# Performance work log

Hardware: AMD Instinct MI355X
Metric: run time of the kernel (lower is better)

Reference implementation:

```python
import jax, jax.numpy as jnp
import numpy as np

BN_EPS = 1e-5


def sparsemax(z):
    # z: [B, D]; sparse projection onto the simplex along last axis.
    D = z.shape[-1]
    z_sorted = jnp.flip(jnp.sort(z, axis=-1), axis=-1)          # descending
    cs = jnp.cumsum(z_sorted, axis=-1)                           # cumulative sums
    k = jnp.arange(1, D + 1, dtype=z.dtype)                      # 1..D
    support = (1.0 + k * z_sorted) > cs                          # support condition
    k_star = jnp.sum(support, axis=-1, keepdims=True)            # support size, int
    cs_k = jnp.take_along_axis(cs, k_star - 1, axis=-1)
    tau = (cs_k - 1.0) / k_star.astype(z.dtype)                  # threshold
    return jnp.maximum(z - tau, 0.0)


def setup_inputs() -> dict:
    key = jax.random.key(0)
    k1, k2, k3 = jax.random.split(key, 3)
    B, D = 32768, 1024
    a = jax.random.normal(k1, (B, D), dtype=jnp.float32)
    p = jax.random.uniform(k2, (B, D), dtype=jnp.float32)        # prior scales in (0,1)
    W = jax.random.normal(k3, (D, D), dtype=jnp.float32) * (1.0 / np.sqrt(D))
    b = jnp.zeros((D,), dtype=jnp.float32)
    gamma = jnp.ones((D,), dtype=jnp.float32)
    beta = jnp.zeros((D,), dtype=jnp.float32)
    return {"a": a, "p": p, "W": W, "b": b, "gamma": gamma, "beta": beta}


def reference(a, p, W, b, gamma, beta):
    # Linear: a @ W^T + b  (torch nn.Linear convention)
    h = jnp.einsum("bd,ed->be", a, W) + b
    # BatchNorm1d (training mode: batch stats, biased variance)
    mean = jnp.mean(h, axis=0)
    var = jnp.mean(jnp.square(h - mean), axis=0)
    h = (h - mean) * jax.lax.rsqrt(var + BN_EPS) * gamma + beta
    # Prior scaling, then sparsemax -> attention mask
    mask = sparsemax(p * h)
    return mask
```

## Files before the change

kernel.cpp:

```cpp
#include <hip/hip_runtime.h>
#include <hip/hip_fp16.h>
#include <stdint.h>

typedef _Float16 f16x8 __attribute__((ext_vector_type(8)));
typedef _Float16 f16x2 __attribute__((ext_vector_type(2)));
typedef float f32x4 __attribute__((ext_vector_type(4)));

#define BM 128
#define BN 128
#define BK 64

__device__ __forceinline__ void async_copy16(const void* g, void* l) {
  __builtin_amdgcn_global_load_lds(
      (__attribute__((address_space(1))) void*)(g),
      (__attribute__((address_space(3))) void*)(l),
      16, 0, 0);
}

__global__ __launch_bounds__(256) void cvt_f32_f16(const float* __restrict__ in,
                                                   _Float16* __restrict__ out,
                                                   size_t n) {
  size_t i = ((size_t)blockIdx.x * 256 + threadIdx.x) * 8;
  if (i + 8 > n) return;
  float4 u = *(const float4*)(in + i);
  float4 v = *(const float4*)(in + i + 4);
  f16x8 h;
  h[0] = (_Float16)u.x; h[1] = (_Float16)u.y; h[2] = (_Float16)u.z; h[3] = (_Float16)u.w;
  h[4] = (_Float16)v.x; h[5] = (_Float16)v.y; h[6] = (_Float16)v.z; h[7] = (_Float16)v.w;
  *(f16x8*)(out + i) = h;
}

template <bool H16>
__global__ __launch_bounds__(256) void gemm_direct(const _Float16* __restrict__ Ah,
                                                   const _Float16* __restrict__ Wh,
                                                   const float* __restrict__ bias,
                                                   void* __restrict__ Hout,
                                                   float* __restrict__ psum,
                                                   float* __restrict__ psumsq,
                                                   int M, int N, int K) {
  __shared__ __attribute__((aligned(16))) _Float16 lsA[BM * BK];
  __shared__ __attribute__((aligned(16))) _Float16 lsB[BN * BK];

  const int tid  = threadIdx.x;
  const int wave = tid >> 6;
  const int lane = tid & 63;
  const int wrow = (wave >> 1) * 64;
  const int wcol = (wave & 1) * 64;
  const int l16  = lane & 15;
  const int quad = lane >> 4;

  const int nx = gridDim.x;
  const int li = blockIdx.y * nx + blockIdx.x;
  const int xcd = li & 7;
  const int jj  = li >> 3;
  const int bnT = jj % nx;
  const int bmT = xcd + (jj / nx) * 8;
  const int bm = bmT * BM;
  const int bn = bnT * BN;

  f32x4 acc[4][4];
#pragma unroll
  for (int i = 0; i < 4; ++i)
#pragma unroll
    for (int j = 0; j < 4; ++j) acc[i][j] = (f32x4){0.f, 0.f, 0.f, 0.f};

  for (int k0 = 0; k0 < K; k0 += BK) {
#pragma unroll
    for (int i = 0; i < 4; ++i) {
      const int basechunk = i * 256 + wave * 64;
      const int g   = basechunk + lane;
      const int row = g >> 3;
      const int kc  = ((g & 7) ^ (row & 7)) << 3;
      async_copy16(Ah + (size_t)(bm + row) * K + k0 + kc, &lsA[basechunk * 8]);
      async_copy16(Wh + (size_t)(bn + row) * K + k0 + kc, &lsB[basechunk * 8]);
    }
    __syncthreads();

#pragma unroll
    for (int kk = 0; kk < BK; kk += 32) {
      f16x8 af[4], bf[4];
#pragma unroll
      for (int i = 0; i < 4; ++i) {
        const int r = wrow + i * 16 + l16;
        const int col = ((kk >> 3) + quad) ^ (l16 & 7);
        af[i] = *(const f16x8*)&lsA[r * 64 + col * 8];
      }
#pragma unroll
      for (int j = 0; j < 4; ++j) {
        const int r = wcol + j * 16 + l16;
        const int col = ((kk >> 3) + quad) ^ (l16 & 7);
        bf[j] = *(const f16x8*)&lsB[r * 64 + col * 8];
      }
#pragma unroll
      for (int i = 0; i < 4; ++i)
#pragma unroll
        for (int j = 0; j < 4; ++j)
          acc[i][j] = __builtin_amdgcn_mfma_f32_16x16x32_f16(af[i], bf[j], acc[i][j], 0, 0, 0);
    }
    __syncthreads();
  }

#pragma unroll
  for (int j = 0; j < 4; ++j) {
    const int c = bn + wcol + j * 16 + l16;
    const float bv = bias[c];
    float s = 0.f, s2 = 0.f;
#pragma unroll
    for (int i = 0; i < 4; ++i) {
      const int r = bm + wrow + i * 16 + quad * 4;
      f32x4 v = acc[i][j];
      const float v0 = v[0] + bv, v1 = v[1] + bv, v2 = v[2] + bv, v3 = v[3] + bv;
      s += v0 + v1 + v2 + v3;
      s2 += v0 * v0 + v1 * v1 + v2 * v2 + v3 * v3;
      if constexpr (H16) {
        f16x2* H2 = (f16x2*)Hout;
        const size_t d0 = (size_t)(r >> 1) * N + c;
        H2[d0]     = (f16x2){(_Float16)v0, (_Float16)v1};
        H2[d0 + N] = (f16x2){(_Float16)v2, (_Float16)v3};
      } else {
        float* Cp = (float*)Hout + (size_t)r * N + c;
        Cp[0] = v0; Cp[(size_t)N] = v1; Cp[2 * (size_t)N] = v2; Cp[3 * (size_t)N] = v3;
      }
    }
    s  += __shfl_xor(s, 16, 64);  s  += __shfl_xor(s, 32, 64);
    s2 += __shfl_xor(s2, 16, 64); s2 += __shfl_xor(s2, 32, 64);
    if (quad == 0) {
      const size_t slot = (size_t)(bmT * 2 + (wave >> 1)) * N + c;
      psum[slot] = s;
      psumsq[slot] = s2;
    }
  }
}

__global__ __launch_bounds__(256) void gemm_fallback(const float* __restrict__ Af,
                                                     const float* __restrict__ Wf,
                                                     const float* __restrict__ bias,
                                                     float* __restrict__ C,
                                                     float* __restrict__ sum,
                                                     float* __restrict__ sumsq,
                                                     int M, int N, int K) {
  __shared__ __attribute__((aligned(16))) _Float16 lsA[BM * BK];
  __shared__ __attribute__((aligned(16))) _Float16 lsB[BN * BK];
  const int tid  = threadIdx.x;
  const int wave = tid >> 6;
  const int lane = tid & 63;
  const int wrow = (wave >> 1) * 64;
  const int wcol = (wave & 1) * 64;
  const int l16  = lane & 15;
  const int quad = lane >> 4;
  const int bm = blockIdx.y * BM;
  const int bn = blockIdx.x * BN;

  f32x4 acc[4][4];
#pragma unroll
  for (int i = 0; i < 4; ++i)
#pragma unroll
    for (int j = 0; j < 4; ++j) acc[i][j] = (f32x4){0.f, 0.f, 0.f, 0.f};

  for (int k0 = 0; k0 < K; k0 += BK) {
#pragma unroll
    for (int i = 0; i < 4; ++i) {
      const int g   = i * 256 + tid;
      const int row = g >> 3;
      const int kc  = ((g & 7) ^ (row & 7)) << 3;
      {
        const float* src = Af + (size_t)(bm + row) * K + k0 + kc;
        float4 u = *(const float4*)src;
        float4 v = *(const float4*)(src + 4);
        f16x8 h;
        h[0] = (_Float16)u.x; h[1] = (_Float16)u.y; h[2] = (_Float16)u.z; h[3] = (_Float16)u.w;
        h[4] = (_Float16)v.x; h[5] = (_Float16)v.y; h[6] = (_Float16)v.z; h[7] = (_Float16)v.w;
        *(f16x8*)&lsA[g * 8] = h;
      }
      {
        const float* src = Wf + (size_t)(bn + row) * K + k0 + kc;
        float4 u = *(const float4*)src;
        float4 v = *(const float4*)(src + 4);
        f16x8 h;
        h[0] = (_Float16)u.x; h[1] = (_Float16)u.y; h[2] = (_Float16)u.z; h[3] = (_Float16)u.w;
        h[4] = (_Float16)v.x; h[5] = (_Float16)v.y; h[6] = (_Float16)v.z; h[7] = (_Float16)v.w;
        *(f16x8*)&lsB[g * 8] = h;
      }
    }
    __syncthreads();
#pragma unroll
    for (int kk = 0; kk < BK; kk += 32) {
      f16x8 af[4], bf[4];
#pragma unroll
      for (int i = 0; i < 4; ++i) {
        const int r = wrow + i * 16 + l16;
        const int col = ((kk >> 3) + quad) ^ (l16 & 7);
        af[i] = *(const f16x8*)&lsA[r * 64 + col * 8];
      }
#pragma unroll
      for (int j = 0; j < 4; ++j) {
        const int r = wcol + j * 16 + l16;
        const int col = ((kk >> 3) + quad) ^ (l16 & 7);
        bf[j] = *(const f16x8*)&lsB[r * 64 + col * 8];
      }
#pragma unroll
      for (int i = 0; i < 4; ++i)
#pragma unroll
        for (int j = 0; j < 4; ++j)
          acc[i][j] = __builtin_amdgcn_mfma_f32_16x16x32_f16(af[i], bf[j], acc[i][j], 0, 0, 0);
    }
    __syncthreads();
  }

#pragma unroll
  for (int j = 0; j < 4; ++j) {
    const int c = bn + wcol + j * 16 + l16;
    const float bv = bias[c];
    float s = 0.f, s2 = 0.f;
#pragma unroll
    for (int i = 0; i < 4; ++i) {
      const int r = bm + wrow + i * 16 + quad * 4;
      float* Cp = C + (size_t)r * N + c;
      f32x4 v = acc[i][j];
#pragma unroll
      for (int rr = 0; rr < 4; ++rr) {
        float val = v[rr] + bv;
        Cp[(size_t)rr * N] = val;
        s += val;
        s2 += val * val;
      }
    }
    s  += __shfl_xor(s, 16, 64);  s  += __shfl_xor(s, 32, 64);
    s2 += __shfl_xor(s2, 16, 64); s2 += __shfl_xor(s2, 32, 64);
    if (quad == 0) {
      atomicAdd(&sum[c], s);
      atomicAdd(&sumsq[c], s2);
    }
  }
}

__global__ __launch_bounds__(256) void bn_finalize_sc(const float* __restrict__ psum,
                                                      const float* __restrict__ psumsq,
                                                      const float* __restrict__ gamma,
                                                      const float* __restrict__ beta,
                                                      float* __restrict__ scale,
                                                      float* __restrict__ shift,
                                                      float invB, int S, int D) {
  const int c = blockIdx.x * 256 + threadIdx.x;
  float s = 0.f, q = 0.f;
  for (int s0 = 0; s0 < S; s0 += 8) {
#pragma unroll
    for (int u = 0; u < 8; ++u) {
      s += psum[(size_t)(s0 + u) * D + c];
      q += psumsq[(size_t)(s0 + u) * D + c];
    }
  }
  float mean = s * invB;
  float var  = q * invB - mean * mean;
  float rstd = rsqrtf(var + 1e-5f);
  float sc = rstd * gamma[c];
  scale[c] = sc;
  shift[c] = beta[c] - mean * sc;
}

__global__ __launch_bounds__(256) void bn_finalize(const float* __restrict__ sum,
                                                   const float* __restrict__ sumsq,
                                                   const float* __restrict__ gamma,
                                                   const float* __restrict__ beta,
                                                   float* __restrict__ scale,
                                                   float* __restrict__ shift,
                                                   float invB) {
  const int c = blockIdx.x * 256 + threadIdx.x;
  float mean = sum[c] * invB;
  float var  = sumsq[c] * invB - mean * mean;
  float rstd = rsqrtf(var + 1e-5f);
  float sc = rstd * gamma[c];
  scale[c] = sc;
  shift[c] = beta[c] - mean * sc;
}

__global__ __launch_bounds__(256) void bn_sparsemax_pair(const _Float16* __restrict__ H2,
                                                         const float* __restrict__ P,
                                                         const float* __restrict__ scale,
                                                         const float* __restrict__ shift,
                                                         float* __restrict__ out, int D) {
  const int wave = threadIdx.x >> 6;
  const int lane = threadIdx.x & 63;
  const int rp = blockIdx.x * 4 + wave;

  const f16x8* Hc = (const f16x8*)(H2 + (size_t)rp * 2 * D);
  const f32x4* P0 = (const f32x4*)(P + (size_t)(2 * rp) * D);
  const f32x4* P1 = (const f32x4*)(P + (size_t)(2 * rp + 1) * D);
  const f32x4* SC = (const f32x4*)scale;
  const f32x4* SH = (const f32x4*)shift;

  f32x4 z0[4], z1[4];
  float tot0 = 0.f, tot1 = 0.f;
#pragma unroll
  for (int j = 0; j < 4; ++j) {
    const int idx = j * 64 + lane;
    f16x8 h = Hc[idx];
    f32x4 h0 = {(float)h[0], (float)h[2], (float)h[4], (float)h[6]};
    f32x4 h1 = {(float)h[1], (float)h[3], (float)h[5], (float)h[7]};
    f32x4 sc = SC[idx], sh = SH[idx];
    f32x4 a0 = P0[idx] * (h0 * sc + sh);
    f32x4 a1 = P1[idx] * (h1 * sc + sh);
    z0[j] = a0; z1[j] = a1;
    tot0 += a0[0] + a0[1] + a0[2] + a0[3];
    tot1 += a1[0] + a1[1] + a1[2] + a1[3];
  }
#pragma unroll
  for (int o = 32; o > 0; o >>= 1) {
    tot0 += __shfl_xor(tot0, o, 64);
    tot1 += __shfl_xor(tot1, o, 64);
  }

  float tau0 = (tot0 - 1.0f) / (float)D;
  float tau1 = (tot1 - 1.0f) / (float)D;
  float k0p = -1.0f, k1p = -1.0f;
  for (int it = 0; it < 64; ++it) {
    float s0 = 0.f, k0 = 0.f, s1 = 0.f, k1 = 0.f;
#pragma unroll
    for (int j = 0; j < 4; ++j)
#pragma unroll
      for (int c = 0; c < 4; ++c) {
        float a = z0[j][c], bv = z1[j][c];
        if (a > tau0)  { s0 += a;  k0 += 1.0f; }
        if (bv > tau1) { s1 += bv; k1 += 1.0f; }
      }
#pragma unroll
    for (int o = 32; o > 0; o >>= 1) {
      s0 += __shfl_xor(s0, o, 64);
      k0 += __shfl_xor(k0, o, 64);
      s1 += __shfl_xor(s1, o, 64);
      k1 += __shfl_xor(k1, o, 64);
    }
    tau0 = (s0 - 1.0f) / k0;
    tau1 = (s1 - 1.0f) / k1;
    if (k0 == k0p && k1 == k1p) break;
    k0p = k0; k1p = k1;
  }

  f32x4* O0 = (f32x4*)(out + (size_t)(2 * rp) * D);
  f32x4* O1 = (f32x4*)(out + (size_t)(2 * rp + 1) * D);
#pragma unroll
  for (int j = 0; j < 4; ++j) {
    const int idx = j * 64 + lane;
    f32x4 o0, o1;
#pragma unroll
    for (int c = 0; c < 4; ++c) {
      o0[c] = fmaxf(z0[j][c] - tau0, 0.f);
      o1[c] = fmaxf(z1[j][c] - tau1, 0.f);
    }
    O0[idx] = o0;
    O1[idx] = o1;
  }
}

__global__ __launch_bounds__(256) void bn_sparsemax_f32(const float* __restrict__ H,
                                                        const float* __restrict__ P,
                                                        const float* __restrict__ scale,
                                                        const float* __restrict__ shift,
                                                        float* __restrict__ out, int D) {
  const int wave = threadIdx.x >> 6;
  const int lane = threadIdx.x & 63;
  const int row = blockIdx.x * 4 + wave;
  const size_t rowoff = (size_t)row * D;
  const f32x4* H4 = (const f32x4*)(H + rowoff);
  const f32x4* P4 = (const f32x4*)(P + rowoff);
  const f32x4* SC = (const f32x4*)scale;
  const f32x4* SH = (const f32x4*)shift;

  f32x4 z[4];
  float tot = 0.f;
#pragma unroll
  for (int j = 0; j < 4; ++j) {
    const int idx = j * 64 + lane;
    f32x4 zz = P4[idx] * (H4[idx] * SC[idx] + SH[idx]);
    z[j] = zz;
    tot += zz[0] + zz[1] + zz[2] + zz[3];
  }
#pragma unroll
  for (int o = 32; o > 0; o >>= 1) tot += __shfl_xor(tot, o, 64);

  float tau = (tot - 1.0f) / (float)D;
  float kprev = -1.0f;
  for (int it = 0; it < 64; ++it) {
    float s = 0.f, kf = 0.f;
#pragma unroll
    for (int j = 0; j < 4; ++j)
#pragma unroll
      for (int c = 0; c < 4; ++c) {
        float zz = z[j][c];
        if (zz > tau) { s += zz; kf += 1.0f; }
      }
#pragma unroll
    for (int o = 32; o > 0; o >>= 1) {
      s  += __shfl_xor(s, o, 64);
      kf += __shfl_xor(kf, o, 64);
    }
    tau = (s - 1.0f) / kf;
    if (kf == kprev) break;
    kprev = kf;
  }

  f32x4* O4 = (f32x4*)(out + rowoff);
#pragma unroll
  for (int j = 0; j < 4; ++j) {
    const int idx = j * 64 + lane;
    f32x4 o;
#pragma unroll
    for (int c = 0; c < 4; ++c) o[c] = fmaxf(z[j][c] - tau, 0.f);
    O4[idx] = o;
  }
}

extern "C" void kernel_launch(void* const* d_in, const int* in_sizes, int n_in,
                              void* d_out, int out_size, void* d_ws, size_t ws_size,
                              hipStream_t stream) {
  const float* a     = (const float*)d_in[0];
  const float* p     = (const float*)d_in[1];
  const float* W     = (const float*)d_in[2];
  const float* b     = (const float*)d_in[3];
  const float* gamma = (const float*)d_in[4];
  const float* beta  = (const float*)d_in[5];
  float* out = (float*)d_out;

  const int D = in_sizes[3];
  const int Brows = in_sizes[0] / D;
  const int K = D, N = D;
  const size_t na = (size_t)Brows * D;
  const size_t nw = (size_t)D * D;
  const int S = (Brows / BM) * 2;

  const size_t statsB = (size_t)D * S * sizeof(float);
  float* psum   = (float*)d_ws;
  float* psumsq = (float*)((char*)d_ws + statsB);
  float* wscale = (float*)((char*)d_ws + 2 * statsB);
  float* wshift = wscale + D;
  const size_t off_Ah = 2 * statsB + 16384;
  _Float16* Ah = (_Float16*)((char*)d_ws + off_Ah);
  _Float16* Wh = Ah + na;
  _Float16* H2 = Wh + nw;
  const size_t need1 = off_Ah + (na + nw) * sizeof(_Float16);
  const size_t need2 = need1 + na * sizeof(_Float16);

  if (ws_size >= need1) {
    cvt_f32_f16<<<dim3((unsigned)(na / 8 / 256)), 256, 0, stream>>>(a, Ah, na);
    cvt_f32_f16<<<dim3((unsigned)(nw / 8 / 256)), 256, 0, stream>>>(W, Wh, nw);
    const bool h16 = ws_size >= need2;
    if (h16) {
      gemm_direct<true><<<dim3(N / BN, Brows / BM), 256, 0, stream>>>(
          Ah, Wh, b, H2, psum, psumsq, Brows, N, K);
    } else {
      gemm_direct<false><<<dim3(N / BN, Brows / BM), 256, 0, stream>>>(
          Ah, Wh, b, out, psum, psumsq, Brows, N, K);
    }
    bn_finalize_sc<<<dim3(D / 256), 256, 0, stream>>>(psum, psumsq, gamma, beta,
                                                      wscale, wshift,
                                                      1.0f / (float)Brows, S, D);
    if (h16) {
      bn_sparsemax_pair<<<dim3(Brows / 8), 256, 0, stream>>>(H2, p, wscale, wshift, out, D);
    } else {
      bn_sparsemax_f32<<<dim3(Brows / 4), 256, 0, stream>>>(out, p, wscale, wshift, out, D);
    }
  } else {
    float* wsum   = (float*)d_ws;
    float* wsumsq = wsum + D;
    float* fscale = wsum + 2 * D;
    float* fshift = wsum + 3 * D;
    hipMemsetAsync(d_ws, 0, 2 * D * sizeof(float), stream);
    gemm_fallback<<<dim3(N / BN, Brows / BM), 256, 0, stream>>>(
        a, W, b, out, wsum, wsumsq, Brows, N, K);
    bn_finalize<<<dim3(D / 256), 256, 0, stream>>>(wsum, wsumsq, gamma, beta, fscale, fshift,
                                                   1.0f / (float)Brows);
    bn_sparsemax_f32<<<dim3(Brows / 4), 256, 0, stream>>>(out, p, fscale, fshift, out, D);
  }
}
```

Measured before the change: 445.8 us.

## Merge conversion launches, parallelize BN finalize per wave, one row per wave sparsemax

Fuses the two f32->f16 conversion launches into one kernel indexed over both arrays. The BN finalize now gives each column its own wave, which reduces the S partial sums with a strided loop plus shuffle reduction instead of a serial loop over S per thread with only 4 blocks. The sparsemax kernel processes one row per wave instead of two interleaved rows. That doubles the number of waves and lets each row's iteration count stop independently, but each wave now reads the full packed f16x8 pairs and uses only half of them.

```diff
diff --git a/kernel.cpp b/kernel.cpp
--- a/kernel.cpp
+++ b/kernel.cpp
@@ -17,11 +17,20 @@
       16, 0, 0);
 }
 
-__global__ __launch_bounds__(256) void cvt_f32_f16(const float* __restrict__ in,
-                                                   _Float16* __restrict__ out,
-                                                   size_t n) {
+__global__ __launch_bounds__(256) void cvt_f32_f16_2(const float* __restrict__ inA, size_t na,
+                                                     const float* __restrict__ inW, size_t nw,
+                                                     _Float16* __restrict__ outA,
+                                                     _Float16* __restrict__ outW) {
   size_t i = ((size_t)blockIdx.x * 256 + threadIdx.x) * 8;
-  if (i + 8 > n) return;
+  const float* in;
+  _Float16* out;
+  if (i < na) {
+    in = inA; out = outA;
+  } else {
+    i -= na;
+    if (i >= nw) return;
+    in = inW; out = outW;
+  }
   float4 u = *(const float4*)(in + i);
   float4 v = *(const float4*)(in + i + 4);
   f16x8 h;
@@ -234,28 +243,34 @@
   }
 }
 
-__global__ __launch_bounds__(256) void bn_finalize_sc(const float* __restrict__ psum,
-                                                      const float* __restrict__ psumsq,
-                                                      const float* __restrict__ gamma,
-                                                      const float* __restrict__ beta,
-                                                      float* __restrict__ scale,
-                                                      float* __restrict__ shift,
-                                                      float invB, int S, int D) {
-  const int c = blockIdx.x * 256 + threadIdx.x;
+__global__ __launch_bounds__(256) void bn_finalize_wave(const float* __restrict__ psum,
+                                                        const float* __restrict__ psumsq,
+                                                        const float* __restrict__ gamma,
+                                                        const float* __restrict__ beta,
+                                                        float* __restrict__ scale,
+                                                        float* __restrict__ shift,
+                                                        float invB, int S, int D) {
+  const int wave = threadIdx.x >> 6;
+  const int lane = threadIdx.x & 63;
+  const int c = blockIdx.x * 4 + wave;
   float s = 0.f, q = 0.f;
-  for (int s0 = 0; s0 < S; s0 += 8) {
-#pragma unroll
-    for (int u = 0; u < 8; ++u) {
-      s += psum[(size_t)(s0 + u) * D + c];
-      q += psumsq[(size_t)(s0 + u) * D + c];
-    }
-  }
-  float mean = s * invB;
-  float var  = q * invB - mean * mean;
-  float rstd = rsqrtf(var + 1e-5f);
-  float sc = rstd * gamma[c];
-  scale[c] = sc;
-  shift[c] = beta[c] - mean * sc;
+  for (int u = lane; u < S; u += 64) {
+    s += psum[(size_t)u * D + c];
+    q += psumsq[(size_t)u * D + c];
+  }
+#pragma unroll
+  for (int o = 32; o > 0; o >>= 1) {
+    s += __shfl_xor(s, o, 64);
+    q += __shfl_xor(q, o, 64);
+  }
+  if (lane == 0) {
+    float mean = s * invB;
+    float var  = q * invB - mean * mean;
+    float rstd = rsqrtf(var + 1e-5f);
+    float sc = rstd * gamma[c];
+    scale[c] = sc;
+    shift[c] = beta[c] - mean * sc;
+  }
 }
 
 __global__ __launch_bounds__(256) void bn_finalize(const float* __restrict__ sum,
@@ -274,81 +289,65 @@
   shift[c] = beta[c] - mean * sc;
 }
 
-__global__ __launch_bounds__(256) void bn_sparsemax_pair(const _Float16* __restrict__ H2,
-                                                         const float* __restrict__ P,
-                                                         const float* __restrict__ scale,
-                                                         const float* __restrict__ shift,
-                                                         float* __restrict__ out, int D) {
+__global__ __launch_bounds__(256) void bn_sparsemax_h2(const _Float16* __restrict__ H2,
+                                                       const float* __restrict__ P,
+                                                       const float* __restrict__ scale,
+                                                       const float* __restrict__ shift,
+                                                       float* __restrict__ out, int D) {
   const int wave = threadIdx.x >> 6;
   const int lane = threadIdx.x & 63;
-  const int rp = blockIdx.x * 4 + wave;
+  const int row = blockIdx.x * 4 + wave;
+  const int rp  = row >> 1;
+  const int par = row & 1;
 
   const f16x8* Hc = (const f16x8*)(H2 + (size_t)rp * 2 * D);
-  const f32x4* P0 = (const f32x4*)(P + (size_t)(2 * rp) * D);
-  const f32x4* P1 = (const f32x4*)(P + (size_t)(2 * rp + 1) * D);
+  const f32x4* P4 = (const f32x4*)(P + (size_t)row * D);
   const f32x4* SC = (const f32x4*)scale;
   const f32x4* SH = (const f32x4*)shift;
 
-  f32x4 z0[4], z1[4];
-  float tot0 = 0.f, tot1 = 0.f;
+  f32x4 z[4];
+  float tot = 0.f;
 #pragma unroll
   for (int j = 0; j < 4; ++j) {
     const int idx = j * 64 + lane;
     f16x8 h = Hc[idx];
-    f32x4 h0 = {(float)h[0], (float)h[2], (float)h[4], (float)h[6]};
-    f32x4 h1 = {(float)h[1], (float)h[3], (float)h[5], (float)h[7]};
-    f32x4 sc = SC[idx], sh = SH[idx];
-    f32x4 a0 = P0[idx] * (h0 * sc + sh);
-    f32x4 a1 = P1[idx] * (h1 * sc + sh);
-    z0[j] = a0; z1[j] = a1;
-    tot0 += a0[0] + a0[1] + a0[2] + a0[3];
-    tot1 += a1[0] + a1[1] + a1[2] + a1[3];
-  }
-#pragma unroll
-  for (int o = 32; o > 0; o >>= 1) {
-    tot0 += __shfl_xor(tot0, o, 64);
-    tot1 += __shfl_xor(tot1, o, 64);
-  }
-
-  float tau0 = (tot0 - 1.0f) / (float)D;
-  float tau1 = (tot1 - 1.0f) / (float)D;
-  float k0p = -1.0f, k1p = -1.0f;
+    f32x4 hv = {(float)h[par], (float)h[2 + par], (float)h[4 + par], (float)h[6 + par]};
+    f32x4 zz = P4[idx] * (hv * SC[idx] + SH[idx]);
+    z[j] = zz;
+    tot += zz[0] + zz[1] + zz[2] + zz[3];
+  }
+#pragma unroll
+  for (int o = 32; o > 0; o >>= 1) tot += __shfl_xor(tot, o, 64);
+
+  float tau = (tot - 1.0f) / (float)D;
+  float kprev = -1.0f;
   for (int it = 0; it < 64; ++it) {
-    float s0 = 0.f, k0 = 0.f, s1 = 0.f, k1 = 0.f;
+    float s = 0.f, kf = 0.f;
 #pragma unroll
     for (int j = 0; j < 4; ++j)
 #pragma unroll
       for (int c = 0; c < 4; ++c) {
-        float a = z0[j][c], bv = z1[j][c];
-        if (a > tau0)  { s0 += a;  k0 += 1.0f; }
-        if (bv > tau1) { s1 += bv; k1 += 1.0f; }
+        float zz = z[j][c];
+        if (zz > tau) { s += zz; kf += 1.0f; }
       }
 #pragma unroll
     for (int o = 32; o > 0; o >>= 1) {
-      s0 += __shfl_xor(s0, o, 64);
-      k0 += __shfl_xor(k0, o, 64);
-      s1 += __shfl_xor(s1, o, 64);
-      k1 += __shfl_xor(k1, o, 64);
-    }
-    tau0 = (s0 - 1.0f) / k0;
-    tau1 = (s1 - 1.0f) / k1;
-    if (k0 == k0p && k1 == k1p) break;
-    k0p = k0; k1p = k1;
-  }
-
-  f32x4* O0 = (f32x4*)(out + (size_t)(2 * rp) * D);
-  f32x4* O1 = (f32x4*)(out + (size_t)(2 * rp + 1) * D);
+      s  += __shfl_xor(s, o, 64);
+      kf += __shfl_xor(kf, o, 64);
+    }
+    tau = (s - 1.0f) / kf;
+    if (kf == kprev) break;
+    kprev = kf;
+  }
+
+  f32x4* O4 = (f32x4*)(out + (size_t)row * D);
 #pragma unroll
   for (int j = 0; j < 4; ++j) {
     const int idx = j * 64 + lane;
-    f32x4 o0, o1;
-#pragma unroll
-    for (int c = 0; c < 4; ++c) {
-      o0[c] = fmaxf(z0[j][c] - tau0, 0.f);
-      o1[c] = fmaxf(z1[j][c] - tau1, 0.f);
-    }
-    O0[idx] = o0;
-    O1[idx] = o1;
+    f32x4 o;
+#pragma unroll
+    for (int c = 0; c < 4; ++c) o[c] = fmaxf(z[j][c] - tau, 0.f);
+    O4[idx] = o;
   }
 }
 
@@ -441,8 +440,8 @@
   const size_t need2 = need1 + na * sizeof(_Float16);
 
   if (ws_size >= need1) {
-    cvt_f32_f16<<<dim3((unsigned)(na / 8 / 256)), 256, 0, stream>>>(a, Ah, na);
-    cvt_f32_f16<<<dim3((unsigned)(nw / 8 / 256)), 256, 0, stream>>>(W, Wh, nw);
+    cvt_f32_f16_2<<<dim3((unsigned)((na + nw) / 8 / 256)), 256, 0, stream>>>(
+        a, na, W, nw, Ah, Wh);
     const bool h16 = ws_size >= need2;
     if (h16) {
       gemm_direct<true><<<dim3(N / BN, Brows / BM), 256, 0, stream>>>(
@@ -451,11 +450,11 @@
       gemm_direct<false><<<dim3(N / BN, Brows / BM), 256, 0, stream>>>(
           Ah, Wh, b, out, psum, psumsq, Brows, N, K);
     }
-    bn_finalize_sc<<<dim3(D / 256), 256, 0, stream>>>(psum, psumsq, gamma, beta,
+    bn_finalize_wave<<<dim3(D / 4), 256, 0, stream>>>(psum, psumsq, gamma, beta,
                                                       wscale, wshift,
                                                       1.0f / (float)Brows, S, D);
     if (h16) {
-      bn_sparsemax_pair<<<dim3(Brows / 8), 256, 0, stream>>>(H2, p, wscale, wshift, out, D);
+      bn_sparsemax_h2<<<dim3(Brows / 4), 256, 0, stream>>>(H2, p, wscale, wshift, out, D);
     } else {
       bn_sparsemax_f32<<<dim3(Brows / 4), 256, 0, stream>>>(out, p, wscale, wshift, out, D);
     }
```

Measured after the change: 424.0 us. 1.05x faster.
